# Performance work log

Measured on AMD Instinct MI355X. Metric: run time of the kernel, lower is better.

## Reference

```python
import jax, jax.numpy as jnp
import numpy as np
import math

NQ = 6        # n_qubits_data
NL = 2        # n_layers (active_layers == n_layers)
K = 3         # unfold kernel
C = 64        # channels
SD = 128      # style_dim
B, H, W = 8, 64, 64
PD = C * K * K  # patch_dim = 576


def _apply_1q(psi, U, w):
    # psi: [bsz, 2,2,...,2]; U: [2,2] or [bsz,2,2]
    psi = jnp.moveaxis(psi, 1 + w, -1)
    if U.ndim == 2:
        psi = jnp.einsum('...j,ij->...i', psi, U)
    else:
        psi = jnp.einsum('b...j,bij->b...i', psi, U)
    return jnp.moveaxis(psi, -1, 1 + w)


def _ry_mat(theta):
    c = jnp.cos(theta / 2)
    s = jnp.sin(theta / 2)
    m = jnp.stack([jnp.stack([c, -s], -1), jnp.stack([s, c], -1)], -2)
    return m.astype(jnp.complex64)


def _rz_mat(theta):
    t = theta.astype(jnp.complex64)
    em = jnp.exp(-0.5j * t)
    ep = jnp.exp(0.5j * t)
    z = jnp.zeros_like(em)
    return jnp.stack([jnp.stack([em, z], -1), jnp.stack([z, ep], -1)], -2)


def _u3_mat(theta, phi, lam):
    t = theta.astype(jnp.complex64)
    p = phi.astype(jnp.complex64)
    l = lam.astype(jnp.complex64)
    ct = jnp.cos(t / 2)
    st = jnp.sin(t / 2)
    return jnp.stack([
        jnp.stack([ct, -jnp.exp(1j * l) * st], -1),
        jnp.stack([jnp.exp(1j * p) * st, jnp.exp(1j * (p + l)) * ct], -1)
    ], -2)


def _cnot(psi, c, t):
    c0, c1 = jnp.split(psi, 2, axis=1 + c)
    c1 = jnp.flip(c1, axis=1 + t)
    return jnp.concatenate([c0, c1], axis=1 + c)


def _forward(x, style, data_proj_w, data_proj_b, style_to_data_w, style_to_data_b,
             qcnn_rot_params, measure_params, out_proj_w, out_proj_b,
             res_proj_w, res_proj_b):
    Bx, Cx, Hx, Wx = x.shape
    # nn.Unfold(3, padding=1): [B, C*9, H*W], channel-major then kernel pos
    xp = jnp.pad(x, ((0, 0), (0, 0), (1, 1), (1, 1)))
    pats = jnp.stack([xp[:, :, i:i + Hx, j:j + Wx]
                      for i in range(K) for j in range(K)], axis=2)  # [B,C,9,H,W]
    patches_flat = pats.reshape(Bx, Cx * K * K, Hx * Wx).transpose(0, 2, 1).reshape(-1, Cx * K * K)
    style_flat = jnp.broadcast_to(style[:, None, :], (Bx, Hx * Wx, style.shape[-1])).reshape(-1, style.shape[-1])

    data_angles = jnp.tanh(patches_flat @ data_proj_w.T + data_proj_b) * math.pi   # [bsz, NQ]
    style_angles = jnp.tanh(style_flat @ style_to_data_w.T + style_to_data_b) * math.pi

    bsz = patches_flat.shape[0]
    psi = jnp.zeros((bsz,) + (2,) * NQ, jnp.complex64)
    psi = psi.at[(slice(None),) + (0,) * NQ].set(1.0)

    # hybrid encoding: RY(data + style) per wire (batched angles)
    theta0 = data_angles + style_angles
    for i in range(NQ):
        psi = _apply_1q(psi, _ry_mat(theta0[:, i]), i)

    # HEA layers: per-wire RY/RZ (scalar params) + ring CNOTs
    for l in range(NL):
        for i in range(NQ):
            psi = _apply_1q(psi, _ry_mat(qcnn_rot_params[l, i, 0, 0]), i)
            psi = _apply_1q(psi, _rz_mat(qcnn_rot_params[l, i, 1, 0]), i)
        for i in range(NQ):
            psi = _cnot(psi, i, (i + 1) % NQ)

    # trainable measurement basis (U3 per wire)
    for i in range(NQ):
        psi = _apply_1q(psi, _u3_mat(measure_params[i, 0], measure_params[i, 1], measure_params[i, 2]), i)

    # PauliZ expvals on all wires
    probs = psi.real ** 2 + psi.imag ** 2
    expvals = []
    for i in range(NQ):
        p = jnp.sum(probs, axis=tuple(a for a in range(1, NQ + 1) if a != 1 + i))  # [bsz,2]
        expvals.append(p[:, 0] - p[:, 1])
    quant_out = jnp.stack(expvals, -1)  # [bsz, NQ]

    out_flat = (quant_out @ out_proj_w.T + out_proj_b) + (patches_flat @ res_proj_w.T + res_proj_b)
    return out_flat.reshape(Bx, Hx, Wx, -1).transpose(0, 3, 1, 2)


def setup_inputs() -> dict:
    key = jax.random.key(0)
    ks = jax.random.split(key, 10)
    return {
        'x': jax.random.normal(ks[0], (B, C, H, W), jnp.float32),
        'style': jax.random.normal(ks[1], (B, SD), jnp.float32),
        'data_proj_w': jax.random.normal(ks[2], (NQ, PD), jnp.float32) * 0.02,
        'data_proj_b': jnp.zeros((NQ,), jnp.float32),
        'style_to_data_w': jax.random.normal(ks[3], (NQ, SD), jnp.float32) * 0.02,
        'style_to_data_b': jnp.zeros((NQ,), jnp.float32),
        'qcnn_rot_params': jax.random.normal(ks[4], (NL, NQ, 2, 3), jnp.float32) * 0.1,
        'measure_params': jax.random.normal(ks[5], (NQ, 3), jnp.float32) * 0.1,
        'out_proj_w': jax.random.normal(ks[6], (C, NQ), jnp.float32) * 0.02,
        'out_proj_b': jnp.zeros((C,), jnp.float32),
        'res_proj_w': jax.random.normal(ks[7], (C, PD), jnp.float32) * 0.02,
        'res_proj_b': jnp.zeros((C,), jnp.float32),
    }


def reference(x, style, data_proj_w, data_proj_b, style_to_data_w, style_to_data_b,
              qcnn_rot_params, measure_params, out_proj_w, out_proj_b,
              res_proj_w, res_proj_b):
    return _forward(x, style, data_proj_w, data_proj_b, style_to_data_w, style_to_data_b,
                    qcnn_rot_params, measure_params, out_proj_w, out_proj_b,
                    res_proj_w, res_proj_b)
```

## Files before the change

kernel.cpp:

```cpp
#include <hip/hip_runtime.h>
#include <hip/hip_cooperative_groups.h>
#include <math.h>

#define PI_F 3.14159265358979323846f

typedef __attribute__((ext_vector_type(8))) short bf16x8;
typedef __attribute__((ext_vector_type(4))) float f32x4;

namespace cg = cooperative_groups;

__device__ float g_sang[48];
__device__ float g_cb[64];
__device__ __attribute__((aligned(16))) unsigned short g_Urb[64 * 64];
__device__ __attribute__((aligned(16))) unsigned short g_Uib[64 * 64];
__device__ __attribute__((aligned(16))) unsigned short g_Zwc[64 * 64];
__device__ __attribute__((aligned(16))) unsigned short g_Bm[5 * 18 * 64 * 8];

__device__ inline unsigned short bf16rne(float f) {
    unsigned u = __float_as_uint(f);
    return (unsigned short)((u + 0x7FFFu + ((u >> 16) & 1u)) >> 16);
}
__device__ inline float rlane(float v, int k) {
    return __uint_as_float(__builtin_amdgcn_readlane(__float_as_uint(v), k));
}

static __device__ void phaseA(const float* __restrict__ style,
                              const float* __restrict__ dw,
                              const float* __restrict__ rw,
                              const float* __restrict__ s2dw,
                              const float* __restrict__ s2db,
                              const float* __restrict__ qcnn,
                              const float* __restrict__ meas,
                              const float* __restrict__ outw,
                              const float* __restrict__ outb,
                              const float* __restrict__ resb) {
    int tid  = threadIdx.x;
    int lane = tid & 63;
    int wid  = tid >> 6;
    int gtid = blockIdx.x * 1024 + tid;

    if (gtid < 5760) {
        int nt   = gtid / 1152;
        int rem  = gtid - nt * 1152;
        int slab = rem >> 6;
        int ln   = rem & 63;
        int mm   = ln & 15, qq = ln >> 4;
        int n    = nt * 16 + mm;
        int ij   = slab >> 1;
        int ch   = (slab & 1) * 32 + qq * 8;
        unsigned pk[4] = {0u, 0u, 0u, 0u};
        if (n < 70) {
            const float* src = (n < 64) ? (rw + n * 576 + ij) : (dw + (n - 64) * 576 + ij);
#pragma unroll
            for (int jj = 0; jj < 4; ++jj) {
                pk[jj] = (unsigned)bf16rne(src[(ch + 2 * jj) * 9])
                       | ((unsigned)bf16rne(src[(ch + 2 * jj + 1) * 9]) << 16);
            }
        }
        *(uint4*)(g_Bm + gtid * 8) = make_uint4(pk[0], pk[1], pk[2], pk[3]);
    }

    if (blockIdx.x == 8) {
        float tsv, tcv;
        {
            int idx = lane < 48 ? lane : 0;
            float arg;
            if (idx < 24) {
                arg = 0.5f * qcnn[idx * 3];
            } else {
                int q3 = (idx - 24) >> 2, part = (idx - 24) & 3;
                float th = meas[q3 * 3 + 0], ph = meas[q3 * 3 + 1], lm = meas[q3 * 3 + 2];
                arg = part == 0 ? 0.5f * th : part == 1 ? lm : part == 2 ? ph : ph + lm;
            }
            sincosf(arg, &tsv, &tcv);
        }
        int s0 = wid * 4;
        float ar[4], ai[4];
#pragma unroll
        for (int cc = 0; cc < 4; ++cc) {
            ar[cc] = (lane == s0 + cc) ? 1.f : 0.f;
            ai[cc] = 0.f;
        }
#pragma unroll
        for (int l = 0; l < 2; ++l) {
#pragma unroll
            for (int wq = 0; wq < 6; ++wq) {
                int mask = 1 << (5 - wq);
                bool hi = (lane & mask) != 0;
                int g = (l * 6 + wq) * 2;
                float sg = rlane(tsv, g),     cg = rlane(tcv, g);
                float sz = rlane(tsv, g + 1), cz = rlane(tcv, g + 1);
                float szz = hi ? sz : -sz;
#pragma unroll
                for (int cc = 0; cc < 4; ++cc) {
                    float pr  = __shfl_xor(ar[cc], mask);
                    float pi2 = __shfl_xor(ai[cc], mask);
                    float nr = hi ? (sg * pr + cg * ar[cc]) : (cg * ar[cc] - sg * pr);
                    float ni = hi ? (sg * pi2 + cg * ai[cc]) : (cg * ai[cc] - sg * pi2);
                    ar[cc] = cz * nr - szz * ni;
                    ai[cc] = cz * ni + szz * nr;
                }
            }
#pragma unroll
            for (int wq = 0; wq < 6; ++wq) {
                int cm = 1 << (5 - wq);
                int tm = 1 << (5 - ((wq + 1) % 6));
#pragma unroll
                for (int cc = 0; cc < 4; ++cc) {
                    float pr  = __shfl_xor(ar[cc], tm);
                    float pi2 = __shfl_xor(ai[cc], tm);
                    if (lane & cm) { ar[cc] = pr; ai[cc] = pi2; }
                }
            }
        }
#pragma unroll
        for (int wq = 0; wq < 6; ++wq) {
            int mask = 1 << (5 - wq);
            bool hi = (lane & mask) != 0;
            int u = 24 + wq * 4;
            float st2 = rlane(tsv, u),     ct  = rlane(tcv, u);
            float sl  = rlane(tsv, u + 1), cl  = rlane(tcv, u + 1);
            float sp  = rlane(tsv, u + 2), cp  = rlane(tcv, u + 2);
            float spl = rlane(tsv, u + 3), cpl = rlane(tcv, u + 3);
            float u01r = -cl * st2, u01i = -sl * st2;
            float u10r =  cp * st2, u10i =  sp * st2;
            float u11r =  cpl * ct, u11i =  spl * ct;
#pragma unroll
            for (int cc = 0; cc < 4; ++cc) {
                float pr  = __shfl_xor(ar[cc], mask);
                float pi2 = __shfl_xor(ai[cc], mask);
                float nr, ni;
                if (hi) {
                    nr = u10r * pr - u10i * pi2 + u11r * ar[cc] - u11i * ai[cc];
                    ni = u10r * pi2 + u10i * pr + u11r * ai[cc] + u11i * ar[cc];
                } else {
                    nr = ct * ar[cc] + u01r * pr - u01i * pi2;
                    ni = ct * ai[cc] + u01r * pi2 + u01i * pr;
                }
                ar[cc] = nr; ai[cc] = ni;
            }
        }
        unsigned short rr[4], ii[4];
#pragma unroll
        for (int cc = 0; cc < 4; ++cc) { rr[cc] = bf16rne(ar[cc]); ii[cc] = bf16rne(ai[cc]); }
        *(uint2*)(g_Urb + lane * 64 + s0) =
            make_uint2((unsigned)rr[0] | ((unsigned)rr[1] << 16),
                       (unsigned)rr[2] | ((unsigned)rr[3] << 16));
        *(uint2*)(g_Uib + lane * 64 + s0) =
            make_uint2((unsigned)ii[0] | ((unsigned)ii[1] << 16),
                       (unsigned)ii[2] | ((unsigned)ii[3] << 16));
    } else if (blockIdx.x == 9) {
        float zr[6];
#pragma unroll
        for (int q = 0; q < 6; ++q) zr[q] = ((lane >> (5 - q)) & 1) ? -1.f : 1.f;
#pragma unroll
        for (int cc = 0; cc < 4; ++cc) {
            int c = wid * 4 + cc;
            float z = 0.f;
#pragma unroll
            for (int q = 0; q < 6; ++q) z += outw[c * 6 + q] * zr[q];
            g_Zwc[c * 64 + lane] = bf16rne(z);
        }
    } else if (blockIdx.x == 10) {
        if (wid == 0) g_cb[lane] = outb[lane] + resb[lane];
        if (wid == 1 && lane < 48) {
            int bb = lane / 6, q = lane % 6;
            float a = s2db[q];
#pragma unroll 8
            for (int j = 0; j < 128; ++j) a += style[bb * 128 + j] * s2dw[q * 128 + j];
            g_sang[lane] = tanhf(a) * PI_F;
        }
    }
}

static __device__ void phaseB(const float* __restrict__ x,
                              const float* __restrict__ dpb,
                              float* __restrict__ out) {
    __shared__ __attribute__((aligned(16))) float smem[13504];
    unsigned*             xsu32 = (unsigned*)smem;
    const unsigned short* xsu   = (const unsigned short*)smem;
    float*          convres = smem + 8320;
    float*          fact    = smem;
    unsigned short* psi_bf  = (unsigned short*)(smem + 1024);
    unsigned short* p_bf    = (unsigned short*)(smem + 3328);

    int tid  = threadIdx.x;
    int lane = tid & 63;
    int wid  = __builtin_amdgcn_readfirstlane(tid >> 6);
    int m    = lane & 15;
    int quad = lane >> 4;

    int p = blockIdx.x * 64 + lane;
    int b = p >> 12;
    int h = (p >> 6) & 63;
    int w = p & 63;
    const float* xb = x + (b << 18);

    if (tid < 216) {
        int r3 = tid / 72, rest = tid % 72;
        int half = rest / 36, cp = rest % 36;
        xsu32[(r3 * 66 + half * 65) * 36 + cp] = 0u;
    }
#pragma unroll
    for (int k = 0; k < 6; ++k) {
        int flat = k * 1024 + tid;
        int row  = flat >> 11;
        int rem  = flat & 2047;
        int cp   = rem >> 6;
        int w2   = rem & 63;
        int hh   = h + row - 1;
        float v0 = 0.f, v1 = 0.f;
        if ((unsigned)hh < 64u) {
            const float* px = xb + (hh << 6) + w2;
            v0 = px[(2 * cp) << 12];
            v1 = px[(2 * cp + 1) << 12];
        }
        xsu32[(row * 66 + w2 + 1) * 36 + cp] =
            (unsigned)bf16rne(v0) | ((unsigned)bf16rne(v1) << 16);
    }
    __syncthreads();

    int mt0 = wid >> 2, nt0 = wid & 3;
    const unsigned short* a0base = xsu + (mt0 * 16 + m) * 72 + quad * 8;
    const unsigned short* b0base = g_Bm + ((nt0 * 18) * 64 + lane) * 8;
    f32x4 acc0 = {0.f, 0.f, 0.f, 0.f};
    f32x4 acc1 = {0.f, 0.f, 0.f, 0.f};
    if (wid < 4) {
        const unsigned short* a1base = xsu + (wid * 16 + m) * 72 + quad * 8;
        const unsigned short* b1base = g_Bm + ((4 * 18) * 64 + lane) * 8;
#pragma unroll
        for (int slab = 0; slab < 18; ++slab) {
            int ij = slab >> 1, i = ij / 3, j = ij - 3 * (ij / 3);
            int aoff = i * 4752 + j * 72 + (slab & 1) * 32;
            bf16x8 a0 = *(const bf16x8*)(a0base + aoff);
            bf16x8 b0 = *(const bf16x8*)(b0base + slab * 512);
            acc0 = __builtin_amdgcn_mfma_f32_16x16x32_bf16(a0, b0, acc0, 0, 0, 0);
            bf16x8 a1 = *(const bf16x8*)(a1base + aoff);
            bf16x8 b1 = *(const bf16x8*)(b1base + slab * 512);
            acc1 = __builtin_amdgcn_mfma_f32_16x16x32_bf16(a1, b1, acc1, 0, 0, 0);
        }
    } else {
#pragma unroll
        for (int slab = 0; slab < 18; ++slab) {
            int ij = slab >> 1, i = ij / 3, j = ij - 3 * (ij / 3);
            int aoff = i * 4752 + j * 72 + (slab & 1) * 32;
            bf16x8 a0 = *(const bf16x8*)(a0base + aoff);
            bf16x8 b0 = *(const bf16x8*)(b0base + slab * 512);
            acc0 = __builtin_amdgcn_mfma_f32_16x16x32_bf16(a0, b0, acc0, 0, 0, 0);
        }
    }
#pragma unroll
    for (int r = 0; r < 4; ++r) {
        convres[(mt0 * 16 + quad * 4 + r) * 81 + nt0 * 16 + m] = acc0[r];
    }
    if (wid < 4) {
#pragma unroll
        for (int r = 0; r < 4; ++r) {
            convres[(wid * 16 + quad * 4 + r) * 81 + 64 + m] = acc1[r];
        }
    }
    __syncthreads();

    if (wid < 6) {
        int q = wid;
        float t = convres[lane * 81 + 64 + q];
        float theta = tanhf(t + dpb[q]) * PI_F + g_sang[b * 6 + q];
        float sv, cv; sincosf(0.5f * theta, &sv, &cv);
        fact[q * 64 + lane] = sv;
        fact[(6 + q) * 64 + lane] = cv;
    }
    __syncthreads();

    {
        float f0s = fact[0 * 64 + lane], f0c = fact[6 * 64 + lane];
        float f1s = fact[1 * 64 + lane], f1c = fact[7 * 64 + lane];
        float f2s = fact[2 * 64 + lane], f2c = fact[8 * 64 + lane];
        float f3s = fact[3 * 64 + lane], f3c = fact[9 * 64 + lane];
        float f4s = fact[4 * 64 + lane], f4c = fact[10 * 64 + lane];
        float f5s = fact[5 * 64 + lane], f5c = fact[11 * 64 + lane];
        int sb = wid * 4;
        float pre = (((sb >> 5) & 1) ? f0s : f0c)
                  * (((sb >> 4) & 1) ? f1s : f1c)
                  * (((sb >> 3) & 1) ? f2s : f2c)
                  * (((sb >> 2) & 1) ? f3s : f3c);
        unsigned short pk[4];
#pragma unroll
        for (int ti = 0; ti < 4; ++ti) {
            float v = pre * ((ti & 2) ? f4s : f4c) * ((ti & 1) ? f5s : f5c);
            pk[ti] = bf16rne(v);
        }
        *(uint2*)(psi_bf + lane * 72 + sb) =
            make_uint2((unsigned)pk[0] | ((unsigned)pk[1] << 16),
                       (unsigned)pk[2] | ((unsigned)pk[3] << 16));
    }
    __syncthreads();

    {
        const unsigned short* pa = psi_bf + (mt0 * 16 + m) * 72 + quad * 8;
        const unsigned short* ur = g_Urb + (nt0 * 16 + m) * 64 + quad * 8;
        const unsigned short* ui = g_Uib + (nt0 * 16 + m) * 64 + quad * 8;
        bf16x8 aA = *(const bf16x8*)(pa);
        bf16x8 aB = *(const bf16x8*)(pa + 32);
        f32x4 c1 = {0.f, 0.f, 0.f, 0.f};
        f32x4 c2 = {0.f, 0.f, 0.f, 0.f};
        c1 = __builtin_amdgcn_mfma_f32_16x16x32_bf16(aA, *(const bf16x8*)(ur), c1, 0, 0, 0);
        c1 = __builtin_amdgcn_mfma_f32_16x16x32_bf16(aB, *(const bf16x8*)(ur + 32), c1, 0, 0, 0);
        c2 = __builtin_amdgcn_mfma_f32_16x16x32_bf16(aA, *(const bf16x8*)(ui), c2, 0, 0, 0);
        c2 = __builtin_amdgcn_mfma_f32_16x16x32_bf16(aB, *(const bf16x8*)(ui + 32), c2, 0, 0, 0);
#pragma unroll
        for (int r = 0; r < 4; ++r) {
            float pv = c1[r] * c1[r] + c2[r] * c2[r];
            p_bf[(mt0 * 16 + quad * 4 + r) * 72 + nt0 * 16 + m] = bf16rne(pv);
        }
    }
    __syncthreads();

    {
        const unsigned short* pa = p_bf + (mt0 * 16 + m) * 72 + quad * 8;
        const unsigned short* zc = g_Zwc + (nt0 * 16 + m) * 64 + quad * 8;
        f32x4 o = {0.f, 0.f, 0.f, 0.f};
        o = __builtin_amdgcn_mfma_f32_16x16x32_bf16(*(const bf16x8*)(pa),
                                                    *(const bf16x8*)(zc), o, 0, 0, 0);
        o = __builtin_amdgcn_mfma_f32_16x16x32_bf16(*(const bf16x8*)(pa + 32),
                                                    *(const bf16x8*)(zc + 32), o, 0, 0, 0);
#pragma unroll
        for (int r = 0; r < 4; ++r) {
            convres[(mt0 * 16 + quad * 4 + r) * 81 + nt0 * 16 + m] += o[r];
        }
    }
    __syncthreads();

    int ob = (b << 18) + (h << 6) + w;
#pragma unroll
    for (int kk = 0; kk < 4; ++kk) {
        int c = wid * 4 + kk;
        out[ob + (c << 12)] = convres[lane * 81 + c] + g_cb[c];
    }
}

__global__ __launch_bounds__(1024, 8) void k_all(
        const float* __restrict__ x,     const float* __restrict__ style,
        const float* __restrict__ dw,    const float* __restrict__ dpb,
        const float* __restrict__ s2dw,  const float* __restrict__ s2db,
        const float* __restrict__ qcnn,  const float* __restrict__ meas,
        const float* __restrict__ outw,  const float* __restrict__ outb,
        const float* __restrict__ rw,    const float* __restrict__ resb,
        float* __restrict__ out) {
    phaseA(style, dw, rw, s2dw, s2db, qcnn, meas, outw, outb, resb);
    __threadfence();
    cg::this_grid().sync();
    phaseB(x, dpb, out);
}

__global__ __launch_bounds__(1024) void k_prep_fb(
        const float* __restrict__ style, const float* __restrict__ dw,
        const float* __restrict__ rw,    const float* __restrict__ s2dw,
        const float* __restrict__ s2db,  const float* __restrict__ qcnn,
        const float* __restrict__ meas,  const float* __restrict__ outw,
        const float* __restrict__ outb,  const float* __restrict__ resb) {
    phaseA(style, dw, rw, s2dw, s2db, qcnn, meas, outw, outb, resb);
}

__global__ __launch_bounds__(1024, 4) void k_main_fb(
        const float* __restrict__ x, const float* __restrict__ dpb,
        float* __restrict__ out) {
    phaseB(x, dpb, out);
}

extern "C" void kernel_launch(void* const* d_in, const int* in_sizes, int n_in,
                              void* d_out, int out_size, void* d_ws, size_t ws_size,
                              hipStream_t stream) {
    const float* x     = (const float*)d_in[0];
    const float* style = (const float*)d_in[1];
    const float* dw    = (const float*)d_in[2];
    const float* dpb   = (const float*)d_in[3];
    const float* s2dw  = (const float*)d_in[4];
    const float* s2db  = (const float*)d_in[5];
    const float* qcnn  = (const float*)d_in[6];
    const float* meas  = (const float*)d_in[7];
    const float* outw  = (const float*)d_in[8];
    const float* outb  = (const float*)d_in[9];
    const float* rw    = (const float*)d_in[10];
    const float* resb  = (const float*)d_in[11];
    float* out = (float*)d_out;

    static int coop_state = -1;
    if (coop_state < 0) {
        int dev = 0;
        hipGetDevice(&dev);
        int attr = 0;
        hipDeviceGetAttribute(&attr, hipDeviceAttributeCooperativeLaunch, dev);
        int ncu = 0;
        hipDeviceGetAttribute(&ncu, hipDeviceAttributeMultiprocessorCount, dev);
        int maxb = 0;
        hipOccupancyMaxActiveBlocksPerMultiprocessor(
            &maxb, reinterpret_cast<const void*>(k_all), 1024, 0);
        coop_state = (attr && (long)maxb * ncu >= 512) ? 1 : 0;
    }

    if (coop_state == 1) {
        void* args[] = {(void*)&x, (void*)&style, (void*)&dw, (void*)&dpb,
                        (void*)&s2dw, (void*)&s2db, (void*)&qcnn, (void*)&meas,
                        (void*)&outw, (void*)&outb, (void*)&rw, (void*)&resb,
                        (void*)&out};
        hipError_t e = hipLaunchCooperativeKernel(
            reinterpret_cast<const void*>(k_all), dim3(512), dim3(1024),
            args, 0, stream);
        if (e == hipSuccess) return;
        coop_state = 0;
    }

    hipLaunchKernelGGL(k_prep_fb, dim3(11), dim3(1024), 0, stream,
                       style, dw, rw, s2dw, s2db, qcnn, meas, outw, outb, resb);
    hipLaunchKernelGGL(k_main_fb, dim3(512), dim3(1024), 0, stream, x, dpb, out);
}
```

Measured before the change: 114.5 us.

## Drop cooperative grid sync and write conv results directly from registers

Replaces the cooperative single-kernel launch and its grid-wide barrier with two plain launches: a small prep kernel that now uses 8 blocks, and the main kernel. The main kernel no longer stages conv/residual results through a large shared-memory buffer. It combines the MFMA accumulators with the quantum-output term and bias in registers and writes float4 directly to global memory. This cuts shared memory per block, which may raise occupancy, and removes a __syncthreads. The cost is an extra kernel launch boundary in place of the in-kernel grid sync, plus output stores whose coalescing pattern differs from before.

```diff
diff --git a/kernel.cpp b/kernel.cpp
--- a/kernel.cpp
+++ b/kernel.cpp
@@ -1,13 +1,10 @@
 #include <hip/hip_runtime.h>
-#include <hip/hip_cooperative_groups.h>
 #include <math.h>
 
 #define PI_F 3.14159265358979323846f
 
 typedef __attribute__((ext_vector_type(8))) short bf16x8;
 typedef __attribute__((ext_vector_type(4))) float f32x4;
-
-namespace cg = cooperative_groups;
 
 __device__ float g_sang[48];
 __device__ float g_cb[64];
@@ -24,132 +21,45 @@
     return __uint_as_float(__builtin_amdgcn_readlane(__float_as_uint(v), k));
 }
 
-static __device__ void phaseA(const float* __restrict__ style,
-                              const float* __restrict__ dw,
-                              const float* __restrict__ rw,
-                              const float* __restrict__ s2dw,
-                              const float* __restrict__ s2db,
-                              const float* __restrict__ qcnn,
-                              const float* __restrict__ meas,
-                              const float* __restrict__ outw,
-                              const float* __restrict__ outb,
-                              const float* __restrict__ resb) {
+__global__ __launch_bounds__(1024) void k_prep(
+        const float* __restrict__ style,
+        const float* __restrict__ dw, const float* __restrict__ rw,
+        const float* __restrict__ s2dw, const float* __restrict__ s2db,
+        const float* __restrict__ qcnn, const float* __restrict__ meas,
+        const float* __restrict__ outw, const float* __restrict__ outb,
+        const float* __restrict__ resb) {
+    int bid  = blockIdx.x;
     int tid  = threadIdx.x;
     int lane = tid & 63;
     int wid  = tid >> 6;
-    int gtid = blockIdx.x * 1024 + tid;
-
-    if (gtid < 5760) {
-        int nt   = gtid / 1152;
-        int rem  = gtid - nt * 1152;
-        int slab = rem >> 6;
-        int ln   = rem & 63;
-        int mm   = ln & 15, qq = ln >> 4;
-        int n    = nt * 16 + mm;
-        int ij   = slab >> 1;
-        int ch   = (slab & 1) * 32 + qq * 8;
-        unsigned pk[4] = {0u, 0u, 0u, 0u};
-        if (n < 70) {
-            const float* src = (n < 64) ? (rw + n * 576 + ij) : (dw + (n - 64) * 576 + ij);
-#pragma unroll
-            for (int jj = 0; jj < 4; ++jj) {
-                pk[jj] = (unsigned)bf16rne(src[(ch + 2 * jj) * 9])
-                       | ((unsigned)bf16rne(src[(ch + 2 * jj + 1) * 9]) << 16);
-            }
-        }
-        *(uint4*)(g_Bm + gtid * 8) = make_uint4(pk[0], pk[1], pk[2], pk[3]);
-    }
-
-    if (blockIdx.x == 8) {
-        float tsv, tcv;
-        {
-            int idx = lane < 48 ? lane : 0;
-            float arg;
-            if (idx < 24) {
-                arg = 0.5f * qcnn[idx * 3];
-            } else {
-                int q3 = (idx - 24) >> 2, part = (idx - 24) & 3;
-                float th = meas[q3 * 3 + 0], ph = meas[q3 * 3 + 1], lm = meas[q3 * 3 + 2];
-                arg = part == 0 ? 0.5f * th : part == 1 ? lm : part == 2 ? ph : ph + lm;
-            }
-            sincosf(arg, &tsv, &tcv);
-        }
-        int s0 = wid * 4;
-        float ar[4], ai[4];
-#pragma unroll
-        for (int cc = 0; cc < 4; ++cc) {
-            ar[cc] = (lane == s0 + cc) ? 1.f : 0.f;
-            ai[cc] = 0.f;
-        }
-#pragma unroll
-        for (int l = 0; l < 2; ++l) {
-#pragma unroll
-            for (int wq = 0; wq < 6; ++wq) {
-                int mask = 1 << (5 - wq);
-                bool hi = (lane & mask) != 0;
-                int g = (l * 6 + wq) * 2;
-                float sg = rlane(tsv, g),     cg = rlane(tcv, g);
-                float sz = rlane(tsv, g + 1), cz = rlane(tcv, g + 1);
-                float szz = hi ? sz : -sz;
-#pragma unroll
-                for (int cc = 0; cc < 4; ++cc) {
-                    float pr  = __shfl_xor(ar[cc], mask);
-                    float pi2 = __shfl_xor(ai[cc], mask);
-                    float nr = hi ? (sg * pr + cg * ar[cc]) : (cg * ar[cc] - sg * pr);
-                    float ni = hi ? (sg * pi2 + cg * ai[cc]) : (cg * ai[cc] - sg * pi2);
-                    ar[cc] = cz * nr - szz * ni;
-                    ai[cc] = cz * ni + szz * nr;
+
+    if (bid >= 1 && bid <= 6) {
+        int entry = (bid - 1) * 1024 + tid;
+        if (entry < 5760) {
+            int nt   = entry / 1152;
+            int rem  = entry - nt * 1152;
+            int slab = rem >> 6;
+            int ln   = rem & 63;
+            int mm   = ln & 15, qq = ln >> 4;
+            int n    = nt * 16 + mm;
+            int ij   = slab >> 1;
+            int ch   = (slab & 1) * 32 + qq * 8;
+            unsigned pk[4] = {0u, 0u, 0u, 0u};
+            if (n < 70) {
+                const float* src = (n < 64) ? (rw + n * 576 + ij)
+                                            : (dw + (n - 64) * 576 + ij);
+#pragma unroll
+                for (int jj = 0; jj < 4; ++jj) {
+                    pk[jj] = (unsigned)bf16rne(src[(ch + 2 * jj) * 9])
+                           | ((unsigned)bf16rne(src[(ch + 2 * jj + 1) * 9]) << 16);
                 }
             }
-#pragma unroll
-            for (int wq = 0; wq < 6; ++wq) {
-                int cm = 1 << (5 - wq);
-                int tm = 1 << (5 - ((wq + 1) % 6));
-#pragma unroll
-                for (int cc = 0; cc < 4; ++cc) {
-                    float pr  = __shfl_xor(ar[cc], tm);
-                    float pi2 = __shfl_xor(ai[cc], tm);
-                    if (lane & cm) { ar[cc] = pr; ai[cc] = pi2; }
-                }
-            }
-        }
-#pragma unroll
-        for (int wq = 0; wq < 6; ++wq) {
-            int mask = 1 << (5 - wq);
-            bool hi = (lane & mask) != 0;
-            int u = 24 + wq * 4;
-            float st2 = rlane(tsv, u),     ct  = rlane(tcv, u);
-            float sl  = rlane(tsv, u + 1), cl  = rlane(tcv, u + 1);
-            float sp  = rlane(tsv, u + 2), cp  = rlane(tcv, u + 2);
-            float spl = rlane(tsv, u + 3), cpl = rlane(tcv, u + 3);
-            float u01r = -cl * st2, u01i = -sl * st2;
-            float u10r =  cp * st2, u10i =  sp * st2;
-            float u11r =  cpl * ct, u11i =  spl * ct;
-#pragma unroll
-            for (int cc = 0; cc < 4; ++cc) {
-                float pr  = __shfl_xor(ar[cc], mask);
-                float pi2 = __shfl_xor(ai[cc], mask);
-                float nr, ni;
-                if (hi) {
-                    nr = u10r * pr - u10i * pi2 + u11r * ar[cc] - u11i * ai[cc];
-                    ni = u10r * pi2 + u10i * pr + u11r * ai[cc] + u11i * ar[cc];
-                } else {
-                    nr = ct * ar[cc] + u01r * pr - u01i * pi2;
-                    ni = ct * ai[cc] + u01r * pi2 + u01i * pr;
-                }
-                ar[cc] = nr; ai[cc] = ni;
-            }
-        }
-        unsigned short rr[4], ii[4];
-#pragma unroll
-        for (int cc = 0; cc < 4; ++cc) { rr[cc] = bf16rne(ar[cc]); ii[cc] = bf16rne(ai[cc]); }
-        *(uint2*)(g_Urb + lane * 64 + s0) =
-            make_uint2((unsigned)rr[0] | ((unsigned)rr[1] << 16),
-                       (unsigned)rr[2] | ((unsigned)rr[3] << 16));
-        *(uint2*)(g_Uib + lane * 64 + s0) =
-            make_uint2((unsigned)ii[0] | ((unsigned)ii[1] << 16),
-                       (unsigned)ii[2] | ((unsigned)ii[3] << 16));
-    } else if (blockIdx.x == 9) {
+            *(uint4*)(g_Bm + entry * 8) = make_uint4(pk[0], pk[1], pk[2], pk[3]);
+        }
+        return;
+    }
+
+    if (bid == 7) {
         float zr[6];
 #pragma unroll
         for (int q = 0; q < 6; ++q) zr[q] = ((lane >> (5 - q)) & 1) ? -1.f : 1.f;
@@ -161,7 +71,6 @@
             for (int q = 0; q < 6; ++q) z += outw[c * 6 + q] * zr[q];
             g_Zwc[c * 64 + lane] = bf16rne(z);
         }
-    } else if (blockIdx.x == 10) {
         if (wid == 0) g_cb[lane] = outb[lane] + resb[lane];
         if (wid == 1 && lane < 48) {
             int bb = lane / 6, q = lane % 6;
@@ -170,19 +79,109 @@
             for (int j = 0; j < 128; ++j) a += style[bb * 128 + j] * s2dw[q * 128 + j];
             g_sang[lane] = tanhf(a) * PI_F;
         }
-    }
-}
-
-static __device__ void phaseB(const float* __restrict__ x,
-                              const float* __restrict__ dpb,
-                              float* __restrict__ out) {
-    __shared__ __attribute__((aligned(16))) float smem[13504];
+        return;
+    }
+
+    float tsv, tcv;
+    {
+        int idx = lane < 48 ? lane : 0;
+        float arg;
+        if (idx < 24) {
+            arg = 0.5f * qcnn[idx * 3];
+        } else {
+            int q3 = (idx - 24) >> 2, part = (idx - 24) & 3;
+            float th = meas[q3 * 3 + 0], ph = meas[q3 * 3 + 1], lm = meas[q3 * 3 + 2];
+            arg = part == 0 ? 0.5f * th : part == 1 ? lm : part == 2 ? ph : ph + lm;
+        }
+        sincosf(arg, &tsv, &tcv);
+    }
+    int s0 = wid * 4;
+    float ar[4], ai[4];
+#pragma unroll
+    for (int cc = 0; cc < 4; ++cc) {
+        ar[cc] = (lane == s0 + cc) ? 1.f : 0.f;
+        ai[cc] = 0.f;
+    }
+#pragma unroll
+    for (int l = 0; l < 2; ++l) {
+#pragma unroll
+        for (int wq = 0; wq < 6; ++wq) {
+            int mask = 1 << (5 - wq);
+            bool hi = (lane & mask) != 0;
+            int g = (l * 6 + wq) * 2;
+            float sg = rlane(tsv, g),     cg = rlane(tcv, g);
+            float sz = rlane(tsv, g + 1), cz = rlane(tcv, g + 1);
+            float szz = hi ? sz : -sz;
+#pragma unroll
+            for (int cc = 0; cc < 4; ++cc) {
+                float pr  = __shfl_xor(ar[cc], mask);
+                float pi2 = __shfl_xor(ai[cc], mask);
+                float nr = hi ? (sg * pr + cg * ar[cc]) : (cg * ar[cc] - sg * pr);
+                float ni = hi ? (sg * pi2 + cg * ai[cc]) : (cg * ai[cc] - sg * pi2);
+                ar[cc] = cz * nr - szz * ni;
+                ai[cc] = cz * ni + szz * nr;
+            }
+        }
+#pragma unroll
+        for (int wq = 0; wq < 6; ++wq) {
+            int cm = 1 << (5 - wq);
+            int tm = 1 << (5 - ((wq + 1) % 6));
+#pragma unroll
+            for (int cc = 0; cc < 4; ++cc) {
+                float pr  = __shfl_xor(ar[cc], tm);
+                float pi2 = __shfl_xor(ai[cc], tm);
+                if (lane & cm) { ar[cc] = pr; ai[cc] = pi2; }
+            }
+        }
+    }
+#pragma unroll
+    for (int wq = 0; wq < 6; ++wq) {
+        int mask = 1 << (5 - wq);
+        bool hi = (lane & mask) != 0;
+        int u = 24 + wq * 4;
+        float st2 = rlane(tsv, u),     ct  = rlane(tcv, u);
+        float sl  = rlane(tsv, u + 1), cl  = rlane(tcv, u + 1);
+        float sp  = rlane(tsv, u + 2), cp  = rlane(tcv, u + 2);
+        float spl = rlane(tsv, u + 3), cpl = rlane(tcv, u + 3);
+        float u01r = -cl * st2, u01i = -sl * st2;
+        float u10r =  cp * st2, u10i =  sp * st2;
+        float u11r =  cpl * ct, u11i =  spl * ct;
+#pragma unroll
+        for (int cc = 0; cc < 4; ++cc) {
+            float pr  = __shfl_xor(ar[cc], mask);
+            float pi2 = __shfl_xor(ai[cc], mask);
+            float nr, ni;
+            if (hi) {
+                nr = u10r * pr - u10i * pi2 + u11r * ar[cc] - u11i * ai[cc];
+                ni = u10r * pi2 + u10i * pr + u11r * ai[cc] + u11i * ar[cc];
+            } else {
+                nr = ct * ar[cc] + u01r * pr - u01i * pi2;
+                ni = ct * ai[cc] + u01r * pi2 + u01i * pr;
+            }
+            ar[cc] = nr; ai[cc] = ni;
+        }
+    }
+    unsigned short rr[4], ii[4];
+#pragma unroll
+    for (int cc = 0; cc < 4; ++cc) { rr[cc] = bf16rne(ar[cc]); ii[cc] = bf16rne(ai[cc]); }
+    *(uint2*)(g_Urb + lane * 64 + s0) =
+        make_uint2((unsigned)rr[0] | ((unsigned)rr[1] << 16),
+                   (unsigned)rr[2] | ((unsigned)rr[3] << 16));
+    *(uint2*)(g_Uib + lane * 64 + s0) =
+        make_uint2((unsigned)ii[0] | ((unsigned)ii[1] << 16),
+                   (unsigned)ii[2] | ((unsigned)ii[3] << 16));
+}
+
+__global__ __launch_bounds__(1024, 8) void k_main(const float* __restrict__ x,
+                                                  const float* __restrict__ dpb,
+                                                  float* __restrict__ out) {
+    __shared__ __attribute__((aligned(16))) float smem[7640];
     unsigned*             xsu32 = (unsigned*)smem;
     const unsigned short* xsu   = (const unsigned short*)smem;
-    float*          convres = smem + 8320;
     float*          fact    = smem;
     unsigned short* psi_bf  = (unsigned short*)(smem + 1024);
     unsigned short* p_bf    = (unsigned short*)(smem + 3328);
+    float*          angs    = smem + 7128;
 
     int tid  = threadIdx.x;
     int lane = tid & 63;
@@ -193,7 +192,6 @@
     int p = blockIdx.x * 64 + lane;
     int b = p >> 12;
     int h = (p >> 6) & 63;
-    int w = p & 63;
     const float* xb = x + (b << 18);
 
     if (tid < 216) {
@@ -249,22 +247,18 @@
             acc0 = __builtin_amdgcn_mfma_f32_16x16x32_bf16(a0, b0, acc0, 0, 0, 0);
         }
     }
-#pragma unroll
-    for (int r = 0; r < 4; ++r) {
-        convres[(mt0 * 16 + quad * 4 + r) * 81 + nt0 * 16 + m] = acc0[r];
-    }
-    if (wid < 4) {
+    if (wid < 4 && m < 6) {
 #pragma unroll
         for (int r = 0; r < 4; ++r) {
-            convres[(wid * 16 + quad * 4 + r) * 81 + 64 + m] = acc1[r];
+            angs[(wid * 16 + quad * 4 + r) * 8 + m] = acc1[r];
         }
     }
     __syncthreads();
 
     if (wid < 6) {
         int q = wid;
-        float t = convres[lane * 81 + 64 + q];
-        float theta = tanhf(t + dpb[q]) * PI_F + g_sang[b * 6 + q];
+        float tv = angs[lane * 8 + q];
+        float theta = tanhf(tv + dpb[q]) * PI_F + g_sang[b * 6 + q];
         float sv, cv; sincosf(0.5f * theta, &sv, &cv);
         fact[q * 64 + lane] = sv;
         fact[(6 + q) * 64 + lane] = cv;
@@ -323,48 +317,16 @@
                                                     *(const bf16x8*)(zc), o, 0, 0, 0);
         o = __builtin_amdgcn_mfma_f32_16x16x32_bf16(*(const bf16x8*)(pa + 32),
                                                     *(const bf16x8*)(zc + 32), o, 0, 0, 0);
-#pragma unroll
-        for (int r = 0; r < 4; ++r) {
-            convres[(mt0 * 16 + quad * 4 + r) * 81 + nt0 * 16 + m] += o[r];
-        }
-    }
-    __syncthreads();
-
-    int ob = (b << 18) + (h << 6) + w;
-#pragma unroll
-    for (int kk = 0; kk < 4; ++kk) {
-        int c = wid * 4 + kk;
-        out[ob + (c << 12)] = convres[lane * 81 + c] + g_cb[c];
-    }
-}
-
-__global__ __launch_bounds__(1024, 8) void k_all(
-        const float* __restrict__ x,     const float* __restrict__ style,
-        const float* __restrict__ dw,    const float* __restrict__ dpb,
-        const float* __restrict__ s2dw,  const float* __restrict__ s2db,
-        const float* __restrict__ qcnn,  const float* __restrict__ meas,
-        const float* __restrict__ outw,  const float* __restrict__ outb,
-        const float* __restrict__ rw,    const float* __restrict__ resb,
-        float* __restrict__ out) {
-    phaseA(style, dw, rw, s2dw, s2db, qcnn, meas, outw, outb, resb);
-    __threadfence();
-    cg::this_grid().sync();
-    phaseB(x, dpb, out);
-}
-
-__global__ __launch_bounds__(1024) void k_prep_fb(
-        const float* __restrict__ style, const float* __restrict__ dw,
-        const float* __restrict__ rw,    const float* __restrict__ s2dw,
-        const float* __restrict__ s2db,  const float* __restrict__ qcnn,
-        const float* __restrict__ meas,  const float* __restrict__ outw,
-        const float* __restrict__ outb,  const float* __restrict__ resb) {
-    phaseA(style, dw, rw, s2dw, s2db, qcnn, meas, outw, outb, resb);
-}
-
-__global__ __launch_bounds__(1024, 4) void k_main_fb(
-        const float* __restrict__ x, const float* __restrict__ dpb,
-        float* __restrict__ out) {
-    phaseB(x, dpb, out);
+        int cch = nt0 * 16 + m;
+        float cbv = g_cb[cch];
+        float4 res;
+        res.x = (acc0[0] + o[0]) + cbv;
+        res.y = (acc0[1] + o[1]) + cbv;
+        res.z = (acc0[2] + o[2]) + cbv;
+        res.w = (acc0[3] + o[3]) + cbv;
+        int base = (b << 18) + (cch << 12) + (h << 6) + mt0 * 16 + quad * 4;
+        *(float4*)(out + base) = res;
+    }
 }
 
 extern "C" void kernel_launch(void* const* d_in, const int* in_sizes, int n_in,
@@ -384,33 +346,7 @@
     const float* resb  = (const float*)d_in[11];
     float* out = (float*)d_out;
 
-    static int coop_state = -1;
-    if (coop_state < 0) {
-        int dev = 0;
-        hipGetDevice(&dev);
-        int attr = 0;
-        hipDeviceGetAttribute(&attr, hipDeviceAttributeCooperativeLaunch, dev);
-        int ncu = 0;
-        hipDeviceGetAttribute(&ncu, hipDeviceAttributeMultiprocessorCount, dev);
-        int maxb = 0;
-        hipOccupancyMaxActiveBlocksPerMultiprocessor(
-            &maxb, reinterpret_cast<const void*>(k_all), 1024, 0);
-        coop_state = (attr && (long)maxb * ncu >= 512) ? 1 : 0;
-    }
-
-    if (coop_state == 1) {
-        void* args[] = {(void*)&x, (void*)&style, (void*)&dw, (void*)&dpb,
-                        (void*)&s2dw, (void*)&s2db, (void*)&qcnn, (void*)&meas,
-                        (void*)&outw, (void*)&outb, (void*)&rw, (void*)&resb,
-                        (void*)&out};
-        hipError_t e = hipLaunchCooperativeKernel(
-            reinterpret_cast<const void*>(k_all), dim3(512), dim3(1024),
-            args, 0, stream);
-        if (e == hipSuccess) return;
-        coop_state = 0;
-    }
-
-    hipLaunchKernelGGL(k_prep_fb, dim3(11), dim3(1024), 0, stream,
+    hipLaunchKernelGGL(k_prep, dim3(8), dim3(1024), 0, stream,
                        style, dw, rw, s2dw, s2db, qcnn, meas, outw, outb, resb);
-    hipLaunchKernelGGL(k_main_fb, dim3(512), dim3(1024), 0, stream, x, dpb, out);
-}
+    hipLaunchKernelGGL(k_main, dim3(512), dim3(1024), 0, stream, x, dpb, out);
+}
```

New measurement: 110.3 us. 3.7% less time.
